# Optimization experiments

Hardware: AMD Instinct MI355X
Metric: run time of the kernel (lower is better)

The kernel has to match this reference:

```python
import jax, jax.numpy as jnp
import numpy as np

B, A, N = 8, 256, 255
NB, NF, NG, NI = 128, 128, 25, 3
MAX_Z = 100
CUTOFF = 5.0
LOG2 = float(np.log(2.0))
EPS = 1e-12


def ssp(x):
    # shifted softplus: ln(0.5*e^x + 0.5)
    return jax.nn.softplus(x) - LOG2


def setup_inputs() -> dict:
    key = jax.random.key(0)
    ks = jax.random.split(key, 12)

    def w(k, shape, fan_in):
        b = 1.0 / np.sqrt(fan_in)
        return jax.random.uniform(k, shape, jnp.float32, -b, b)

    embedding = jax.random.normal(ks[0], (MAX_Z, NB), jnp.float32) * 0.1
    embedding = embedding.at[0].set(0.0)  # padding_idx=0

    inp = dict(
        atomic_numbers=jax.random.randint(ks[6], (B, A), 1, MAX_Z),
        positions=jax.random.normal(ks[7], (B, A, 3), jnp.float32) * 3.0,
        neighbors=jax.random.randint(ks[8], (B, A, N), 0, A),
        neighbor_mask=jnp.ones((B, A, N), jnp.float32),
        embedding=embedding,
        # filter-generating network (per interaction block)
        fw1=w(ks[1], (NI, NG, NF), NG), fb1=jnp.zeros((NI, NF), jnp.float32),
        fw2=w(ks[2], (NI, NF, NF), NF), fb2=jnp.zeros((NI, NF), jnp.float32),
        # cfconv in2f (no bias), f2out, and output dense
        in2f=w(ks[3], (NI, NB, NF), NB),
        f2out_w=w(ks[4], (NI, NF, NB), NF), f2out_b=jnp.zeros((NI, NB), jnp.float32),
        dense_w=w(ks[5], (NI, NB, NB), NB), dense_b=jnp.zeros((NI, NB), jnp.float32),
    )
    return inp


def _schnet_forward(atomic_numbers, positions, neighbors, neighbor_mask, embedding,
                    fw1, fb1, fw2, fb2, in2f, f2out_w, f2out_b, dense_w, dense_b):
    # atom embeddings [B, A, NB]
    x = embedding[atomic_numbers]

    gather = jax.vmap(lambda t, idx: t[idx])  # per-molecule gather along atom axis

    # AtomDistances: r_ij [B, A, N]
    nbr_pos = gather(positions, neighbors)            # [B, A, N, 3]
    dist_vec = nbr_pos - positions[:, :, None, :]
    r_ij = jnp.sqrt(jnp.sum(dist_vec * dist_vec, -1) + EPS)
    r_ij = r_ij * neighbor_mask                       # zero masked distances

    # GaussianSmearing: f_ij [B, A, N, NG]
    offsets = jnp.linspace(0.0, CUTOFF, NG, dtype=jnp.float32)
    width = offsets[1] - offsets[0]
    coeff = -0.5 / (width * width)
    f_ij = jnp.exp(coeff * (r_ij[..., None] - offsets) ** 2)

    # CosineCutoff [B, A, N]
    C = 0.5 * (jnp.cos(r_ij * (np.pi / CUTOFF)) + 1.0) * (r_ij < CUTOFF).astype(x.dtype)

    for i in range(NI):
        # filter network on expanded distances -> W [B, A, N, NF]
        W = ssp(jnp.einsum('bang,gf->banf', f_ij, fw1[i]) + fb1[i])
        W = jnp.einsum('banf,fg->bang', W, fw2[i]) + fb2[i]
        W = W * C[..., None]
        # cfconv: project, gather neighbors, filter, aggregate
        y = jnp.einsum('bad,df->baf', x, in2f[i])      # [B, A, NF]
        y_nbr = gather(y, neighbors)                   # [B, A, N, NF]
        agg = jnp.sum(y_nbr * W * neighbor_mask[..., None], axis=2)  # [B, A, NF]
        v = ssp(jnp.einsum('baf,fd->bad', agg, f2out_w[i]) + f2out_b[i])
        v = jnp.einsum('bad,de->bae', v, dense_w[i]) + dense_b[i]
        x = x + v
    return x


def reference(atomic_numbers, positions, neighbors, neighbor_mask, embedding,
              fw1, fb1, fw2, fb2, in2f, f2out_w, f2out_b, dense_w, dense_b):
    return _schnet_forward(atomic_numbers, positions, neighbors, neighbor_mask, embedding,
                           fw1, fb1, fw2, fb2, in2f, f2out_w, f2out_b, dense_w, dense_b)
```

## Files before the change

kernel.cpp:

```cpp
#include <hip/hip_runtime.h>


#define NATOM 2048
#define NNBR  255

typedef __attribute__((ext_vector_type(8))) short bf16x8;
typedef __attribute__((ext_vector_type(4))) float f32x4;

__device__ __forceinline__ unsigned short f2bf(float x){
  unsigned int u = __float_as_uint(x);
  u += 0x7fffu + ((u >> 16) & 1u);
  return (unsigned short)(u >> 16);
}

__device__ __forceinline__ float sspf(float x){
  return __logf(fmaf(0.5f, __expf(x), 0.5f));
}

__global__ void k_embed(const int* __restrict__ Z, const float* __restrict__ emb,
                        float* __restrict__ x){
  const int atom = blockIdx.x, t = threadIdx.x;
  x[atom*128 + t] = emb[Z[atom]*128 + t];
}

__global__ void k_prep(const float* __restrict__ pos, const int* __restrict__ nbr,
                       const float* __restrict__ mask,
                       float* __restrict__ r_c, float* __restrict__ S_c,
                       int* __restrict__ nb_c, int* __restrict__ nact_g){
  __shared__ int wcnt[4];
  const int n = threadIdx.x, atom = blockIdx.x, molBase = atom & ~255;
  const int wid = n >> 6, lane = n & 63;
  float r = 0.f, S = 0.f; int nb = 0;
  if (n < NNBR){
    nb = nbr[atom*NNBR + n];
    const float ax = pos[atom*3+0], ay = pos[atom*3+1], az = pos[atom*3+2];
    const int pi = (molBase + nb)*3;
    const float dx = pos[pi+0]-ax, dy = pos[pi+1]-ay, dz = pos[pi+2]-az;
    r = sqrtf(dx*dx + dy*dy + dz*dz + 1e-12f);
    const float m = mask[atom*NNBR + n];
    r *= m;
    const float C = (r < 5.0f) ? 0.5f*(__cosf(r*0.6283185307179586f)+1.0f) : 0.f;
    S = C * m;
  }
  r_c[atom*256 + n] = 0.f; S_c[atom*256 + n] = 0.f; nb_c[atom*256 + n] = 0;
  const unsigned long long b = __ballot(S != 0.f);
  const int rank = __popcll(b & ((1ull << lane) - 1ull));
  if (lane == 0) wcnt[wid] = __popcll(b);
  __syncthreads();
  int off = 0;
  for (int w = 0; w < 4; ++w) if (w < wid) off += wcnt[w];
  if (S != 0.f){
    const int slot = off + rank;
    r_c[atom*256 + slot] = r; S_c[atom*256 + slot] = S; nb_c[atom*256 + slot] = nb;
  }
  if (n == 0) nact_g[atom] = wcnt[0] + wcnt[1] + wcnt[2] + wcnt[3];
}

__global__ void k_prepw(const float* __restrict__ fw1, const float* __restrict__ fw2,
                        unsigned short* __restrict__ b1f, unsigned short* __restrict__ b2f){
  const int i = blockIdx.x, tid = threadIdx.x;
  const float* w1 = fw1 + i*25*128;
  const float* w2 = fw2 + i*128*128;
  unsigned short* o1 = b1f + i*8*64*8;
  unsigned short* o2 = b2f + i*32*64*8;
  for (int idx = tid; idx < 8*64; idx += 256){
    const int n = idx >> 6, l = idx & 63, khi = l >> 4, llo = l & 15;
    for (int j = 0; j < 8; ++j){
      const int g = khi*8 + j;
      o1[idx*8 + j] = f2bf((g < 25) ? w1[g*128 + n*16 + llo] : 0.f);
    }
  }
  for (int idx = tid; idx < 32*64; idx += 256){
    const int frag = idx >> 6, l = idx & 63;
    const int k0 = frag >> 3, n = frag & 7, khi = l >> 4, llo = l & 15;
    for (int j = 0; j < 8; ++j){
      const int k = k0*32 + khi*8 + j;
      o2[idx*8 + j] = f2bf(w2[k*128 + n*16 + llo]);
    }
  }
}

__global__ void k_y(const float* __restrict__ x, const float* __restrict__ w,
                    float* __restrict__ y){
  __shared__ float xs[128];
  const int t = threadIdx.x, atom = blockIdx.x;
  xs[t] = x[atom*128 + t];
  __syncthreads();
  float acc = 0.f;
  #pragma unroll 8
  for (int d = 0; d < 128; ++d) acc += xs[d] * w[d*128 + t];
  y[atom*128 + t] = acc;
}

__global__ __launch_bounds__(256, 3) void k_pairs(
    const float* __restrict__ r_c, const float* __restrict__ S_c,
    const int* __restrict__ nb_c, const int* __restrict__ nact_g,
    const float* __restrict__ y,
    const unsigned short* __restrict__ b1f, const unsigned short* __restrict__ b2f,
    const float* __restrict__ fb1, const float* __restrict__ fb2,
    const float* __restrict__ w_f2out, const float* __restrict__ b_f2out,
    const float* __restrict__ w_dense, const float* __restrict__ b_dense,
    float* __restrict__ x){
  __shared__ __align__(16) char smem[51200];
  unsigned short* B2s = (unsigned short*)smem;
  float* red  = (float*)(smem + 32768);
  float* aggL = (float*)(smem + 49152);
  float* po   = (float*)(smem + 49152 + 512);
  float* v1L  = (float*)(smem + 49152 + 1536);

  const int tid = threadIdx.x;
  const int wid = tid >> 6, lane = tid & 63, lhi = lane >> 4, llo = lane & 15;
  const int atom = blockIdx.x, molBase = atom & ~255;
  char* Hw = smem + 32768 + wid*4096;

  {
    const float4* src = (const float4*)b2f;
    float4* dst = (float4*)B2s;
    #pragma unroll
    for (int k = 0; k < 8; ++k) dst[k*256 + tid] = src[k*256 + tid];
  }
  bf16x8 B1[8];
  #pragma unroll
  for (int n = 0; n < 8; ++n) B1[n] = *(const bf16x8*)(b1f + (n*64 + lane)*8);
  float b1b[8], b2b[8];
  #pragma unroll
  for (int n = 0; n < 8; ++n){ b1b[n] = fb1[n*16 + llo]; b2b[n] = fb2[n*16 + llo]; }

  const int nact = nact_g[atom];
  const int ntiles = (nact + 15) >> 4;

  float aggp[8];
  #pragma unroll
  for (int n = 0; n < 8; ++n) aggp[n] = 0.f;

  const float STEP = 5.0f/24.0f;
  const float GC   = -11.52f;
  const f32x4 zero4 = {0.f,0.f,0.f,0.f};

  __syncthreads();

  for (int t = wid; t < ntiles; t += 4){
    const int row0 = t*16;
    const float r = r_c[atom*256 + row0 + llo];
    bf16x8 a1;
    #pragma unroll
    for (int jj = 0; jj < 8; ++jj){
      const int g = lhi*8 + jj;
      float v = 0.f;
      if (g < 25){ const float d = r - (float)g*STEP; v = __expf(GC*d*d); }
      a1[jj] = (short)f2bf(v);
    }
    f32x4 h[8];
    #pragma unroll
    for (int n = 0; n < 8; ++n)
      h[n] = __builtin_amdgcn_mfma_f32_16x16x32_bf16(a1, B1[n], zero4, 0, 0, 0);
    #pragma unroll
    for (int n = 0; n < 8; ++n)
      #pragma unroll
      for (int j = 0; j < 4; ++j){
        const int lrow = 4*lhi + j;
        const float hv = sspf(h[n][j] + b1b[n]);
        const int boff = (lrow*256 + (n*16 + llo)*2) ^ ((lrow & 7) << 4);
        *(unsigned short*)(Hw + boff) = f2bf(hv);
      }
    f32x4 acc[8];
    #pragma unroll
    for (int n = 0; n < 8; ++n) acc[n] = zero4;
    #pragma unroll
    for (int k0 = 0; k0 < 4; ++k0){
      const int boff = (llo*256 + k0*64 + lhi*16) ^ ((llo & 7) << 4);
      const bf16x8 a2 = *(const bf16x8*)(Hw + boff);
      #pragma unroll
      for (int n = 0; n < 8; ++n){
        const bf16x8 b2 = *(const bf16x8*)(B2s + ((k0*8 + n)*64 + lane)*8);
        acc[n] = __builtin_amdgcn_mfma_f32_16x16x32_bf16(a2, b2, acc[n], 0, 0, 0);
      }
    }
    #pragma unroll
    for (int j = 0; j < 4; ++j){
      const int grow = row0 + 4*lhi + j;
      const float S = S_c[atom*256 + grow];
      const float* yrow = y + (molBase + nb_c[atom*256 + grow])*128;
      #pragma unroll
      for (int n = 0; n < 8; ++n)
        aggp[n] = fmaf((acc[n][j] + b2b[n]) * S, yrow[n*16 + llo], aggp[n]);
    }
  }

  __syncthreads();
  #pragma unroll
  for (int n = 0; n < 8; ++n) red[(wid*4 + lhi)*128 + n*16 + llo] = aggp[n];
  __syncthreads();
  if (tid < 128){
    float s = 0.f;
    #pragma unroll
    for (int k = 0; k < 16; ++k) s += red[k*128 + tid];
    aggL[tid] = s;
  }
  __syncthreads();

  {
    const int f = tid & 127, hh = tid >> 7;
    float a1v = 0.f;
    #pragma unroll 8
    for (int t2 = 0; t2 < 64; ++t2){
      const int hidx = hh*64 + t2;
      a1v += aggL[hidx] * w_f2out[hidx*128 + f];
    }
    po[tid] = a1v;
    __syncthreads();
    if (tid < 128) v1L[tid] = sspf(po[tid] + po[tid + 128] + b_f2out[tid]);
    __syncthreads();
    float a2v = 0.f;
    #pragma unroll 8
    for (int t2 = 0; t2 < 64; ++t2){
      const int d = hh*64 + t2;
      a2v += v1L[d] * w_dense[d*128 + f];
    }
    po[tid] = a2v;
    __syncthreads();
    if (tid < 128) x[atom*128 + tid] += po[tid] + po[tid + 128] + b_dense[tid];
  }
}

extern "C" void kernel_launch(void* const* d_in, const int* in_sizes, int n_in,
                              void* d_out, int out_size, void* d_ws, size_t ws_size,
                              hipStream_t stream){
  const int*   Z    = (const int*)  d_in[0];
  const float* pos  = (const float*)d_in[1];
  const int*   nbr  = (const int*)  d_in[2];
  const float* mask = (const float*)d_in[3];
  const float* emb  = (const float*)d_in[4];
  const float* fw1  = (const float*)d_in[5];
  const float* fb1  = (const float*)d_in[6];
  const float* fw2  = (const float*)d_in[7];
  const float* fb2  = (const float*)d_in[8];
  const float* in2f = (const float*)d_in[9];
  const float* f2w  = (const float*)d_in[10];
  const float* f2b  = (const float*)d_in[11];
  const float* dw   = (const float*)d_in[12];
  const float* db   = (const float*)d_in[13];
  float* x = (float*)d_out;

  char* ws = (char*)d_ws;
  float* y    = (float*)ws;
  float* r_c  = (float*)(ws + 1*1024*1024);
  float* S_c  = (float*)(ws + 3*1024*1024);
  int*   nb_c = (int*)  (ws + 5*1024*1024);
  int*   nact = (int*)  (ws + 7*1024*1024);
  unsigned short* b1f = (unsigned short*)(ws + 7*1024*1024 + 16*1024);
  unsigned short* b2f = b1f + 3*8*64*8;

  k_embed<<<NATOM, 128, 0, stream>>>(Z, emb, x);
  k_prep <<<NATOM, 256, 0, stream>>>(pos, nbr, mask, r_c, S_c, nb_c, nact);
  k_prepw<<<3,     256, 0, stream>>>(fw1, fw2, b1f, b2f);
  for (int i = 0; i < 3; ++i){
    k_y    <<<NATOM, 128, 0, stream>>>(x, in2f + i*128*128, y);
    k_pairs<<<NATOM, 256, 0, stream>>>(r_c, S_c, nb_c, nact, y,
        b1f + i*8*64*8, b2f + i*32*64*8,
        fb1 + i*128, fb2 + i*128,
        f2w + i*128*128, f2b + i*128, dw + i*128*128, db + i*128, x);
  }
}
```

Baseline: 173.8 us.

## Split pair and MLP stages, map one atom per wave, fuse next projection

k_pairs now assigns one atom to each wave, so a block of four waves covers four atoms. Each wave reduces its aggregate with shuffles and writes it to a global agg buffer, which removes the shared-memory reduction and the per-atom dense tail. A new k_mlp kernel applies f2out, ssp and dense, updates x, and computes the next layer's in2f projection in the same launch. The embedding lookup is fused with the first projection, and the weights are pre-transposed so their loads can be float4. The trade-off is extra global traffic for agg, the B2 staging in shared memory is amortised over four atoms per block, and launch bounds drop to 2 blocks per CU.

```diff
diff --git a/kernel.cpp b/kernel.cpp
--- a/kernel.cpp
+++ b/kernel.cpp
@@ -15,12 +15,6 @@
 
 __device__ __forceinline__ float sspf(float x){
   return __logf(fmaf(0.5f, __expf(x), 0.5f));
-}
-
-__global__ void k_embed(const int* __restrict__ Z, const float* __restrict__ emb,
-                        float* __restrict__ x){
-  const int atom = blockIdx.x, t = threadIdx.x;
-  x[atom*128 + t] = emb[Z[atom]*128 + t];
 }
 
 __global__ void k_prep(const float* __restrict__ pos, const int* __restrict__ nbr,
@@ -57,7 +51,10 @@
 }
 
 __global__ void k_prepw(const float* __restrict__ fw1, const float* __restrict__ fw2,
-                        unsigned short* __restrict__ b1f, unsigned short* __restrict__ b2f){
+                        const float* __restrict__ f2w, const float* __restrict__ dw,
+                        const float* __restrict__ in2f,
+                        unsigned short* __restrict__ b1f, unsigned short* __restrict__ b2f,
+                        float* __restrict__ wT){
   const int i = blockIdx.x, tid = threadIdx.x;
   const float* w1 = fw1 + i*25*128;
   const float* w2 = fw2 + i*128*128;
@@ -78,39 +75,96 @@
       o2[idx*8 + j] = f2bf(w2[k*128 + n*16 + llo]);
     }
   }
-}
-
-__global__ void k_y(const float* __restrict__ x, const float* __restrict__ w,
-                    float* __restrict__ y){
+  for (int m = 0; m < 3; ++m){
+    const float* src = (m == 0 ? f2w : (m == 1 ? dw : in2f)) + i*16384;
+    float* dst = wT + (i*3 + m)*16384;
+    for (int idx = tid; idx < 16384; idx += 256){
+      const int r = idx >> 7, c = idx & 127;
+      dst[c*128 + r] = src[idx];
+    }
+  }
+}
+
+__global__ void k_init(const int* __restrict__ Z, const float* __restrict__ emb,
+                       const float* __restrict__ in2fT,
+                       float* __restrict__ x, float* __restrict__ y){
   __shared__ float xs[128];
   const int t = threadIdx.x, atom = blockIdx.x;
-  xs[t] = x[atom*128 + t];
+  const float v = emb[Z[atom]*128 + t];
+  x[atom*128 + t] = v; xs[t] = v;
   __syncthreads();
   float acc = 0.f;
+  const float4* w4 = (const float4*)(in2fT + t*128);
   #pragma unroll 8
-  for (int d = 0; d < 128; ++d) acc += xs[d] * w[d*128 + t];
+  for (int d4 = 0; d4 < 32; ++d4){
+    const float4 w = w4[d4];
+    acc = fmaf(xs[d4*4+0], w.x, acc); acc = fmaf(xs[d4*4+1], w.y, acc);
+    acc = fmaf(xs[d4*4+2], w.z, acc); acc = fmaf(xs[d4*4+3], w.w, acc);
+  }
   y[atom*128 + t] = acc;
 }
 
-__global__ __launch_bounds__(256, 3) void k_pairs(
+__global__ void k_mlp(const float* __restrict__ agg,
+                      const float* __restrict__ f2outT, const float* __restrict__ b_f2out,
+                      const float* __restrict__ denseT, const float* __restrict__ b_dense,
+                      const float* __restrict__ in2fT_next,
+                      float* __restrict__ x, float* __restrict__ y){
+  __shared__ float aggL[128], v1[128], xs[128];
+  const int t = threadIdx.x, atom = blockIdx.x;
+  aggL[t] = agg[atom*128 + t];
+  __syncthreads();
+  float a = 0.f;
+  {
+    const float4* w4 = (const float4*)(f2outT + t*128);
+    #pragma unroll 8
+    for (int d4 = 0; d4 < 32; ++d4){
+      const float4 w = w4[d4];
+      a = fmaf(aggL[d4*4+0], w.x, a); a = fmaf(aggL[d4*4+1], w.y, a);
+      a = fmaf(aggL[d4*4+2], w.z, a); a = fmaf(aggL[d4*4+3], w.w, a);
+    }
+  }
+  v1[t] = sspf(a + b_f2out[t]);
+  __syncthreads();
+  float b = 0.f;
+  {
+    const float4* w4 = (const float4*)(denseT + t*128);
+    #pragma unroll 8
+    for (int d4 = 0; d4 < 32; ++d4){
+      const float4 w = w4[d4];
+      b = fmaf(v1[d4*4+0], w.x, b); b = fmaf(v1[d4*4+1], w.y, b);
+      b = fmaf(v1[d4*4+2], w.z, b); b = fmaf(v1[d4*4+3], w.w, b);
+    }
+  }
+  const float xn = x[atom*128 + t] + b + b_dense[t];
+  x[atom*128 + t] = xn;
+  if (in2fT_next){
+    xs[t] = xn;
+    __syncthreads();
+    float yv = 0.f;
+    const float4* w4 = (const float4*)(in2fT_next + t*128);
+    #pragma unroll 8
+    for (int d4 = 0; d4 < 32; ++d4){
+      const float4 w = w4[d4];
+      yv = fmaf(xs[d4*4+0], w.x, yv); yv = fmaf(xs[d4*4+1], w.y, yv);
+      yv = fmaf(xs[d4*4+2], w.z, yv); yv = fmaf(xs[d4*4+3], w.w, yv);
+    }
+    y[atom*128 + t] = yv;
+  }
+}
+
+__global__ __launch_bounds__(256, 2) void k_pairs(
     const float* __restrict__ r_c, const float* __restrict__ S_c,
     const int* __restrict__ nb_c, const int* __restrict__ nact_g,
     const float* __restrict__ y,
     const unsigned short* __restrict__ b1f, const unsigned short* __restrict__ b2f,
     const float* __restrict__ fb1, const float* __restrict__ fb2,
-    const float* __restrict__ w_f2out, const float* __restrict__ b_f2out,
-    const float* __restrict__ w_dense, const float* __restrict__ b_dense,
-    float* __restrict__ x){
-  __shared__ __align__(16) char smem[51200];
+    float* __restrict__ agg){
+  __shared__ __align__(16) char smem[49152];
   unsigned short* B2s = (unsigned short*)smem;
-  float* red  = (float*)(smem + 32768);
-  float* aggL = (float*)(smem + 49152);
-  float* po   = (float*)(smem + 49152 + 512);
-  float* v1L  = (float*)(smem + 49152 + 1536);
 
   const int tid = threadIdx.x;
   const int wid = tid >> 6, lane = tid & 63, lhi = lane >> 4, llo = lane & 15;
-  const int atom = blockIdx.x, molBase = atom & ~255;
+  const int atom = blockIdx.x*4 + wid, molBase = atom & ~255;
   char* Hw = smem + 32768 + wid*4096;
 
   {
@@ -139,7 +193,7 @@
 
   __syncthreads();
 
-  for (int t = wid; t < ntiles; t += 4){
+  for (int t = 0; t < ntiles; ++t){
     const int row0 = t*16;
     const float r = r_c[atom*256 + row0 + llo];
     bf16x8 a1;
@@ -172,8 +226,8 @@
       const bf16x8 a2 = *(const bf16x8*)(Hw + boff);
       #pragma unroll
       for (int n = 0; n < 8; ++n){
-        const bf16x8 b2 = *(const bf16x8*)(B2s + ((k0*8 + n)*64 + lane)*8);
-        acc[n] = __builtin_amdgcn_mfma_f32_16x16x32_bf16(a2, b2, acc[n], 0, 0, 0);
+        const bf16x8 b2v = *(const bf16x8*)(B2s + ((k0*8 + n)*64 + lane)*8);
+        acc[n] = __builtin_amdgcn_mfma_f32_16x16x32_bf16(a2, b2v, acc[n], 0, 0, 0);
       }
     }
     #pragma unroll
@@ -187,39 +241,14 @@
     }
   }
 
-  __syncthreads();
-  #pragma unroll
-  for (int n = 0; n < 8; ++n) red[(wid*4 + lhi)*128 + n*16 + llo] = aggp[n];
-  __syncthreads();
-  if (tid < 128){
-    float s = 0.f;
-    #pragma unroll
-    for (int k = 0; k < 16; ++k) s += red[k*128 + tid];
-    aggL[tid] = s;
-  }
-  __syncthreads();
-
-  {
-    const int f = tid & 127, hh = tid >> 7;
-    float a1v = 0.f;
-    #pragma unroll 8
-    for (int t2 = 0; t2 < 64; ++t2){
-      const int hidx = hh*64 + t2;
-      a1v += aggL[hidx] * w_f2out[hidx*128 + f];
-    }
-    po[tid] = a1v;
-    __syncthreads();
-    if (tid < 128) v1L[tid] = sspf(po[tid] + po[tid + 128] + b_f2out[tid]);
-    __syncthreads();
-    float a2v = 0.f;
-    #pragma unroll 8
-    for (int t2 = 0; t2 < 64; ++t2){
-      const int d = hh*64 + t2;
-      a2v += v1L[d] * w_dense[d*128 + f];
-    }
-    po[tid] = a2v;
-    __syncthreads();
-    if (tid < 128) x[atom*128 + tid] += po[tid] + po[tid + 128] + b_dense[tid];
+  #pragma unroll
+  for (int n = 0; n < 8; ++n){
+    aggp[n] += __shfl_xor(aggp[n], 16);
+    aggp[n] += __shfl_xor(aggp[n], 32);
+  }
+  if (lane < 16){
+    #pragma unroll
+    for (int n = 0; n < 8; ++n) agg[atom*128 + n*16 + lane] = aggp[n];
   }
 }
 
@@ -244,21 +273,24 @@
 
   char* ws = (char*)d_ws;
   float* y    = (float*)ws;
-  float* r_c  = (float*)(ws + 1*1024*1024);
-  float* S_c  = (float*)(ws + 3*1024*1024);
-  int*   nb_c = (int*)  (ws + 5*1024*1024);
-  int*   nact = (int*)  (ws + 7*1024*1024);
-  unsigned short* b1f = (unsigned short*)(ws + 7*1024*1024 + 16*1024);
-  unsigned short* b2f = b1f + 3*8*64*8;
-
-  k_embed<<<NATOM, 128, 0, stream>>>(Z, emb, x);
+  float* agg  = (float*)(ws + 1*1024*1024);
+  float* r_c  = (float*)(ws + 2*1024*1024);
+  float* S_c  = (float*)(ws + 4*1024*1024);
+  int*   nb_c = (int*)  (ws + 6*1024*1024);
+  int*   nact = (int*)  (ws + 8*1024*1024);
+  unsigned short* b1f = (unsigned short*)(ws + 8*1024*1024 + 16*1024);
+  unsigned short* b2f = (unsigned short*)(ws + 8*1024*1024 + 64*1024);
+  float* wT = (float*)(ws + 8*1024*1024 + 256*1024);
+
+  k_prepw<<<3,     256, 0, stream>>>(fw1, fw2, f2w, dw, in2f, b1f, b2f, wT);
   k_prep <<<NATOM, 256, 0, stream>>>(pos, nbr, mask, r_c, S_c, nb_c, nact);
-  k_prepw<<<3,     256, 0, stream>>>(fw1, fw2, b1f, b2f);
+  k_init <<<NATOM, 128, 0, stream>>>(Z, emb, wT + 2*16384, x, y);
   for (int i = 0; i < 3; ++i){
-    k_y    <<<NATOM, 128, 0, stream>>>(x, in2f + i*128*128, y);
-    k_pairs<<<NATOM, 256, 0, stream>>>(r_c, S_c, nb_c, nact, y,
-        b1f + i*8*64*8, b2f + i*32*64*8,
-        fb1 + i*128, fb2 + i*128,
-        f2w + i*128*128, f2b + i*128, dw + i*128*128, db + i*128, x);
-  }
-}
+    k_pairs<<<NATOM/4, 256, 0, stream>>>(r_c, S_c, nb_c, nact, y,
+        b1f + i*8*64*8, b2f + i*32*64*8, fb1 + i*128, fb2 + i*128, agg);
+    k_mlp  <<<NATOM, 128, 0, stream>>>(agg,
+        wT + (i*3+0)*16384, f2b + i*128,
+        wT + (i*3+1)*16384, db  + i*128,
+        (i < 2) ? (wT + ((i+1)*3+2)*16384) : nullptr, x, y);
+  }
+}
```

Measured after the change: 302.6 us. 1.74x slower.
